# Optimization experiments

Hardware: AMD Instinct MI355X
Metric: run time of the kernel (lower is better)

Reference implementation:

```python
import jax, jax.numpy as jnp
import numpy as np

H = 8
NUM_GRAPHS = 128
EDGE_DIM = 147

def _glorot(k, shape, fan_in):
    return jax.random.normal(k, shape, jnp.float32) * (1.0 / np.sqrt(fan_in))

def setup_inputs():
    ks = jax.random.split(jax.random.key(0), 28)
    N, E = 50000, 200000
    inp = {}
    inp['x'] = jax.random.normal(ks[0], (N, 64), jnp.float32)
    inp['edge_attr'] = jax.random.uniform(ks[1], (E, EDGE_DIM), dtype=jnp.float32)
    dims = [(64, 64), (512, 64), (512, 32)]  # (in_channels, per-head out) per GATConv layer
    ki = 2
    for i in range(3):
        cin, c = dims[i]
        hc = H * c
        inp['W%d' % i] = _glorot(ks[ki], (hc, cin), cin); ki += 1
        inp['We%d' % i] = _glorot(ks[ki], (hc, EDGE_DIM), EDGE_DIM); ki += 1
        inp['as%d' % i] = _glorot(ks[ki], (1, H, c), c); ki += 1
        inp['ad%d' % i] = _glorot(ks[ki], (1, H, c), c); ki += 1
        inp['ae%d' % i] = _glorot(ks[ki], (1, H, c), c); ki += 1
        inp['b%d' % i] = jnp.zeros((hc,), jnp.float32); ki += 1
    inp['Wc'] = _glorot(ks[ki], (32, 256), 256)
    inp['bc'] = jnp.zeros((32,), jnp.float32)
    inp['edge_index'] = jax.random.randint(ks[ki + 1], (2, E), 0, N)
    inp['batch'] = jnp.sort(jax.random.randint(ks[ki + 2], (N,), 0, NUM_GRAPHS))
    return inp

def _gat_layer(x, src, dst, ea, W, We, a_s, a_d, a_e, b):
    # PyG GATConv (concat=True, eval mode): project, per-edge attention logits,
    # softmax over incoming edges of each destination node, weighted scatter-sum, bias.
    N = x.shape[0]
    HC = W.shape[0]
    C = HC // H
    xp = (x @ W.T).reshape(N, H, C)              # [N,H,C]
    ep = (ea @ We.T).reshape(-1, H, C)           # [E,H,C]
    logits = (xp * a_s).sum(-1)[src] + (xp * a_d).sum(-1)[dst] + (ep * a_e).sum(-1)
    logits = jax.nn.leaky_relu(logits, 0.2)      # [E,H]
    mx = jax.ops.segment_max(logits, dst, num_segments=N)
    mx = jnp.where(jnp.isfinite(mx), mx, 0.0)
    ex = jnp.exp(logits - mx[dst])
    denom = jax.ops.segment_sum(ex, dst, num_segments=N)
    attn = ex / (denom[dst] + 1e-16)             # [E,H]
    out = jax.ops.segment_sum(xp[src] * attn[:, :, None], dst, num_segments=N)
    return out.reshape(N, HC) + b

def _forward(x, edge_attr, params, Wc, bc, edge_index, batch):
    N = x.shape[0]
    src, dst = edge_index[0], edge_index[1]
    # GATConv add_self_loops=True, fill_value='mean': self-loop edge attr is
    # the per-node mean of incoming edge attrs (0 for isolated nodes).
    ones_e = jnp.ones((src.shape[0],), x.dtype)
    deg = jax.ops.segment_sum(ones_e, dst, num_segments=N)
    loop_attr = jax.ops.segment_sum(edge_attr, dst, num_segments=N) / jnp.clip(deg, 1.0)[:, None]
    ar = jnp.arange(N)
    src_f = jnp.concatenate([src, ar])
    dst_f = jnp.concatenate([dst, ar])
    ea_f = jnp.concatenate([edge_attr, loop_attr], axis=0)
    h = x
    for i, p in enumerate(params):
        h = _gat_layer(h, src_f, dst_f, ea_f, *p)
        if i < len(params) - 1:
            h = jax.nn.elu(h)  # dropout is identity in eval
    # batch indices are sorted and contiguous, so the unique->contiguous remap
    # in the original forward is the identity; global mean pool:
    cnt = jax.ops.segment_sum(jnp.ones((N,), h.dtype), batch, num_segments=NUM_GRAPHS)
    pooled = jax.ops.segment_sum(h, batch, num_segments=NUM_GRAPHS) / jnp.clip(cnt, 1.0)[:, None]
    return pooled @ Wc.T + bc

def reference(x, edge_attr, W0, We0, as0, ad0, ae0, b0, W1, We1, as1, ad1, ae1, b1, W2, We2, as2, ad2, ae2, b2, Wc, bc, edge_index, batch):
    params = [(W0, We0, as0, ad0, ae0, b0), (W1, We1, as1, ad1, ae1, b1), (W2, We2, as2, ad2, ae2, b2)]
    return _forward(x, edge_attr, params, Wc, bc, edge_index, batch)
```

## Files before the change

kernel.cpp:

```cpp
#include <hip/hip_runtime.h>
#include <hip/hip_bf16.h>
#include <math.h>

typedef __attribute__((ext_vector_type(8))) _Float16 f16x8;
typedef __attribute__((ext_vector_type(4))) _Float16 f16x4;
typedef __attribute__((ext_vector_type(4))) float f32x4;

#define AS1(p) ((const __attribute__((address_space(1))) void*)(p))
#define AS3(p) ((__attribute__((address_space(3))) void*)(p))

__device__ __forceinline__ float leaky02(float x){ return x > 0.f ? x : 0.2f*x; }
__device__ __forceinline__ ushort f2h(float f){ _Float16 h = (_Float16)f; return *(ushort*)&h; }
__device__ __forceinline__ float h2f(ushort u){ _Float16 h = *(_Float16*)&u; return (float)h; }

__global__ void count_kernel(const int* __restrict__ dst, int* __restrict__ cnt, int E){
  int e = blockIdx.x*blockDim.x + threadIdx.x;
  if (e < E) atomicAdd(&cnt[dst[e]], 1);
}

__global__ void scanA_kernel(const int* __restrict__ cnt, int* __restrict__ bsum, int N){
  __shared__ int sd[256];
  int i = blockIdx.x*256 + threadIdx.x;
  sd[threadIdx.x] = (i<N) ? cnt[i] : 0;
  __syncthreads();
  for (int off=128; off>0; off>>=1){
    if (threadIdx.x < off) sd[threadIdx.x] += sd[threadIdx.x+off];
    __syncthreads();
  }
  if (threadIdx.x==0) bsum[blockIdx.x] = sd[0];
}
__global__ void scanB_kernel(int* __restrict__ bsum, int B){
  __shared__ int sd[256];
  int t = threadIdx.x;
  int v = (t<B) ? bsum[t] : 0;
  sd[t] = v;
  __syncthreads();
  for (int off=1; off<256; off<<=1){
    int u = (t>=off) ? sd[t-off] : 0;
    __syncthreads();
    sd[t] += u;
    __syncthreads();
  }
  if (t<B) bsum[t] = sd[t] - v;
}
__global__ void scanC_kernel(const int* __restrict__ cnt, const int* __restrict__ bsum,
                             int* __restrict__ row_ptr, int N){
  __shared__ int sd[256];
  int i = blockIdx.x*256 + threadIdx.x;
  int v = (i<N) ? cnt[i] : 0;
  sd[threadIdx.x] = v;
  __syncthreads();
  for (int off=1; off<256; off<<=1){
    int u = (threadIdx.x>=off) ? sd[threadIdx.x-off] : 0;
    __syncthreads();
    sd[threadIdx.x] += u;
    __syncthreads();
  }
  if (i < N) row_ptr[i+1] = sd[threadIdx.x] + bsum[blockIdx.x];
  if (i == 0) row_ptr[0] = 0;
}

__global__ void scatter_kernel(const int* __restrict__ src, const int* __restrict__ dst,
                               const int* __restrict__ row_ptr, int* __restrict__ cursor,
                               int* __restrict__ epos, int* __restrict__ csr_src,
                               int* __restrict__ csr_dst, int E){
  int e = blockIdx.x*blockDim.x + threadIdx.x;
  if (e < E){
    int d = dst[e];
    int pos = row_ptr[d] + atomicAdd(&cursor[d], 1);
    epos[e] = pos;
    csr_src[pos] = src[e];
    csr_dst[pos] = d;
  }
}

__global__ void conv4_kernel(const float* __restrict__ p0, const float* __restrict__ p1,
                             const float* __restrict__ p2, const float* __restrict__ p3,
                             ushort* __restrict__ q0, ushort* __restrict__ q1,
                             ushort* __restrict__ q2, ushort* __restrict__ q3,
                             int n0, int n1, int n2, int n3){
  int i = blockIdx.x*256 + threadIdx.x;
  const float* src; ushort* dst; int loc;
  if (i < n0){ src=p0; dst=q0; loc=i; }
  else if (i < n0+n1){ src=p1; dst=q1; loc=i-n0; }
  else if (i < n0+n1+n2){ src=p2; dst=q2; loc=i-n0-n1; }
  else if (i < n0+n1+n2+n3){ src=p3; dst=q3; loc=i-n0-n1-n2; }
  else return;
  float4 v = reinterpret_cast<const float4*>(src)[loc];
  ushort4 o; o.x=f2h(v.x); o.y=f2h(v.y); o.z=f2h(v.z); o.w=f2h(v.w);
  reinterpret_cast<ushort4*>(dst)[loc] = o;
}

__global__ void wfold_direct_kernel(const float* __restrict__ We0, const float* __restrict__ ae0,
                                    const float* __restrict__ We1, const float* __restrict__ ae1,
                                    const float* __restrict__ We2, const float* __restrict__ ae2,
                                    ushort* __restrict__ Bh){
  int t = blockIdx.x*256 + threadIdx.x;
  if (t >= 32*160) return;
  int j = t/160, d = t%160;
  float s = 0.f;
  if (j < 24 && d < 147){
    int l = j >> 3, h = j & 7;
    const float* We = (l==0) ? We0 : (l==1) ? We1 : We2;
    const float* ae = (l==0) ? ae0 : (l==1) ? ae1 : ae2;
    int C = (l==2) ? 32 : 64;
    for (int c=0;c<C;c++) s = fmaf(We[(size_t)(h*C+c)*147 + d], ae[h*C+c], s);
  }
  Bh[t] = f2h(s);
}

__global__ __launch_bounds__(256) void edge_alpha_mfma_kernel(const float* __restrict__ ea, const ushort* __restrict__ Bh,
                                                              const int* __restrict__ epos,
                                                              float* __restrict__ aEc, int E){
  int wave = threadIdx.x>>6, lane = threadIdx.x&63;
  int fr = lane&15, fq = lane>>4;
  int m0 = blockIdx.x*64 + wave*16;
  f32x4 acc0 = {0.f,0.f,0.f,0.f}, acc1 = {0.f,0.f,0.f,0.f};
  int row = m0 + fr; if (row > E-1) row = E-1;
  const float*  ar = ea + (size_t)row*147;
  const ushort* b0 = Bh + (size_t)fr*160      + fq*8;
  const ushort* b1 = Bh + (size_t)(16+fr)*160 + fq*8;
  #pragma unroll
  for (int k=0;k<160;k+=32){
    int c0 = k + fq*8;
    f16x8 a;
    #pragma unroll
    for (int u=0;u<8;u++){
      float v = (c0+u < 147) ? ar[c0+u] : 0.f;
      a[u] = (_Float16)v;
    }
    f16x8 p = *(const f16x8*)(b0 + k);
    f16x8 q = *(const f16x8*)(b1 + k);
    acc0 = __builtin_amdgcn_mfma_f32_16x16x32_f16(a, p, acc0, 0, 0, 0);
    acc1 = __builtin_amdgcn_mfma_f32_16x16x32_f16(a, q, acc1, 0, 0, 0);
  }
  #pragma unroll
  for (int j=0;j<4;j++){
    int r = m0 + fq*4 + j;
    if (r < E){
      int p = epos[r];
      aEc[(size_t)p*24 + fr] = acc0[j];
      if (fr < 8) aEc[(size_t)p*24 + 16 + fr] = acc1[j];
    }
  }
}

__global__ __launch_bounds__(192) void loop_alpha_all_kernel(const float* __restrict__ aEc, const int* __restrict__ row_ptr,
                                                             float* __restrict__ loopAE, int N){
  int n = blockIdx.x*8 + threadIdx.x/24;
  int j = threadIdx.x%24;
  if (n >= N) return;
  int row = row_ptr[n], end = row_ptr[n+1];
  float s = 0.f;
  for (int i=row;i<end;i++) s += aEc[(size_t)i*24 + j];
  loopAE[(size_t)n*24 + j] = s / fmaxf((float)(end-row), 1.0f);
}

__global__ __launch_bounds__(256) void edge_exp_kernel(
    const float* __restrict__ alphaS, const float* __restrict__ alphaD,
    const float* __restrict__ aEc, const float* __restrict__ loopAE,
    const int* __restrict__ csr_src, const int* __restrict__ csr_dst,
    float* __restrict__ exv_csr, float* __restrict__ selfEx,
    int E, int N, int off){
  int t = blockIdx.x*256 + threadIdx.x;
  if (t < E*8){
    int i = t >> 3, h = t & 7;
    int s = csr_src[i], n = csr_dst[i];
    float v = leaky02(alphaS[(size_t)s*8+h] + alphaD[(size_t)n*8+h] + aEc[(size_t)i*24 + off + h]);
    exv_csr[t] = __expf(v);
  } else if (t < (E+N)*8){
    int u = t - E*8;
    int n = u >> 3, h = u & 7;
    float v = leaky02(alphaS[(size_t)n*8+h] + alphaD[(size_t)n*8+h] + loopAE[(size_t)n*24 + off + h]);
    selfEx[u] = __expf(v);
  }
}

template<int CPH>
__global__ __launch_bounds__(256) void gemm_mfma_kernel(const ushort* __restrict__ A, const ushort* __restrict__ B,
                                                        ushort* __restrict__ C,
                                                        const float* __restrict__ a_s, const float* __restrict__ a_d,
                                                        float* __restrict__ alphaS, float* __restrict__ alphaD,
                                                        int M, int Nn, int K, int NY){
  __shared__ ushort lds[128*64*4];
  int nwg = gridDim.x;
  int bid = blockIdx.x;
  int q8 = nwg >> 3, r8 = nwg & 7;
  int xcd = bid & 7, loc = bid >> 3;
  int swz = (xcd < r8 ? xcd*(q8+1) : r8*(q8+1) + (xcd-r8)*q8) + loc;
  int m0 = (swz / NY) * 128, n0 = (swz % NY) * 128;

  int wave = threadIdx.x >> 6, lane = threadIdx.x & 63;
  int wr = wave >> 1, wc = wave & 1;
  f32x4 acc[4][4];
  #pragma unroll
  for (int m=0;m<4;m++)
    #pragma unroll
    for (int n=0;n<4;n++) acc[m][n] = (f32x4){0.f,0.f,0.f,0.f};

  int lrow = lane >> 3;
  int lcol = lane & 7;
  int srcChunk = lcol ^ lrow;
  int fr = lane & 15;
  int fq = lane >> 4;

  auto stage = [&](int buf, int k0){
    ushort* As = lds + buf*(128*64*2);
    ushort* Bs = As + 128*64;
    #pragma unroll
    for (int qq=0;qq<4;qq++){
      int r = qq*32 + wave*8 + lrow;
      int gr = m0 + r; if (gr > M-1) gr = M-1;
      __builtin_amdgcn_global_load_lds(AS1(A + (size_t)gr*K + k0 + srcChunk*8), AS3(&As[(qq*32 + wave*8)*64]), 16, 0, 0);
      __builtin_amdgcn_global_load_lds(AS1(B + (size_t)(n0 + r)*K + k0 + srcChunk*8), AS3(&Bs[(qq*32 + wave*8)*64]), 16, 0, 0);
    }
  };

  int nt = K >> 6;
  stage(0, 0);
  int buf = 0;
  for (int t=0; t<nt; ++t){
    if (t+1 < nt){
      stage(buf^1, (t+1)<<6);
      asm volatile("s_waitcnt vmcnt(8)" ::: "memory");
    } else {
      asm volatile("s_waitcnt vmcnt(0)" ::: "memory");
    }
    __builtin_amdgcn_s_barrier();
    __builtin_amdgcn_sched_barrier(0);
    const ushort* As = lds + buf*(128*64*2);
    const ushort* Bs = As + 128*64;
    #pragma unroll
    for (int kk=0; kk<64; kk+=32){
      f16x8 a[4], b[4];
      #pragma unroll
      for (int m=0;m<4;m++){
        int Ra = wr*64 + m*16 + fr;
        int ch = ((kk>>3) + fq) ^ (Ra & 7);
        a[m] = *(const f16x8*)&As[Ra*64 + ch*8];
      }
      #pragma unroll
      for (int n=0;n<4;n++){
        int Rb = wc*64 + n*16 + fr;
        int ch = ((kk>>3) + fq) ^ (Rb & 7);
        b[n] = *(const f16x8*)&Bs[Rb*64 + ch*8];
      }
      #pragma unroll
      for (int m=0;m<4;m++)
        #pragma unroll
        for (int n=0;n<4;n++)
          acc[m][n] = __builtin_amdgcn_mfma_f32_16x16x32_f16(a[m], b[n], acc[m][n], 0, 0, 0);
    }
    __builtin_amdgcn_s_barrier();
    buf ^= 1;
  }

  {
    ushort* Cs = lds;
    #pragma unroll
    for (int m=0;m<4;m++)
      #pragma unroll
      for (int j=0;j<4;j++){
        int rr = wr*64 + m*16 + fq*4 + j;
        #pragma unroll
        for (int n=0;n<4;n++)
          Cs[rr*128 + wc*64 + n*16 + fr] = f2h(acc[m][n][j]);
      }
    __builtin_amdgcn_s_barrier();
    int rbase = threadIdx.x >> 4;
    int cc = (threadIdx.x & 15)*8;
    #pragma unroll
    for (int p=0;p<8;p++){
      int rr = p*16 + rbase;
      int grow = m0 + rr;
      if (grow < M)
        *(f16x8*)(C + (size_t)grow*Nn + n0 + cc) = *(const f16x8*)&Cs[rr*128 + cc];
    }
  }

  int colbase = n0 + wc*64;
  if (CPH == 64){
    int head = colbase >> 6;
    float asv[4], adv[4];
    #pragma unroll
    for (int n=0;n<4;n++){ int cih = n*16 + fr; asv[n] = a_s[head*64 + cih]; adv[n] = a_d[head*64 + cih]; }
    #pragma unroll
    for (int m=0;m<4;m++){
      float ps[4] = {0,0,0,0}, pd[4] = {0,0,0,0};
      #pragma unroll
      for (int n=0;n<4;n++)
        #pragma unroll
        for (int j=0;j<4;j++){ ps[j] = fmaf(acc[m][n][j], asv[n], ps[j]); pd[j] = fmaf(acc[m][n][j], adv[n], pd[j]); }
      #pragma unroll
      for (int off=1; off<16; off<<=1)
        #pragma unroll
        for (int j=0;j<4;j++){ ps[j] += __shfl_xor(ps[j], off); pd[j] += __shfl_xor(pd[j], off); }
      if (fr == 0){
        #pragma unroll
        for (int j=0;j<4;j++){
          int row = m0 + wr*64 + m*16 + fq*4 + j;
          if (row < M){ alphaS[(size_t)row*8 + head] = ps[j]; alphaD[(size_t)row*8 + head] = pd[j]; }
        }
      }
    }
  } else {
    int head0 = colbase >> 5;
    float asv[4], adv[4];
    #pragma unroll
    for (int n=0;n<4;n++){
      int h = head0 + (n>>1);
      int cih = (n&1)*16 + fr;
      asv[n] = a_s[h*32 + cih]; adv[n] = a_d[h*32 + cih];
    }
    #pragma unroll
    for (int m=0;m<4;m++){
      float psA[4]={0,0,0,0}, pdA[4]={0,0,0,0}, psB[4]={0,0,0,0}, pdB[4]={0,0,0,0};
      #pragma unroll
      for (int j=0;j<4;j++){
        #pragma unroll
        for (int n=0;n<2;n++){ psA[j] = fmaf(acc[m][n][j], asv[n], psA[j]); pdA[j] = fmaf(acc[m][n][j], adv[n], pdA[j]); }
        #pragma unroll
        for (int n=2;n<4;n++){ psB[j] = fmaf(acc[m][n][j], asv[n], psB[j]); pdB[j] = fmaf(acc[m][n][j], adv[n], pdB[j]); }
      }
      #pragma unroll
      for (int off=1; off<16; off<<=1)
        #pragma unroll
        for (int j=0;j<4;j++){
          psA[j] += __shfl_xor(psA[j], off); pdA[j] += __shfl_xor(pdA[j], off);
          psB[j] += __shfl_xor(psB[j], off); pdB[j] += __shfl_xor(pdB[j], off);
        }
      if (fr == 0){
        #pragma unroll
        for (int j=0;j<4;j++){
          int row = m0 + wr*64 + m*16 + fq*4 + j;
          if (row < M){
            alphaS[(size_t)row*8 + head0]     = psA[j]; alphaD[(size_t)row*8 + head0]     = pdA[j];
            alphaS[(size_t)row*8 + head0 + 1] = psB[j]; alphaD[(size_t)row*8 + head0 + 1] = pdB[j];
          }
        }
      }
    }
  }
}

template<int V>
__device__ __forceinline__ void rowfma(const ushort* p, float ex, float* acc){
  if (V == 8){
    f16x8 v = *(const f16x8*)p;
    #pragma unroll
    for (int j=0;j<8;j++) acc[j] = fmaf(ex, (float)v[j], acc[j]);
  } else {
    f16x4 v = *(const f16x4*)p;
    #pragma unroll
    for (int j=0;j<V;j++) acc[j] = fmaf(ex, (float)v[j], acc[j]);
  }
}

template<int HC, int ELU>
__global__ __launch_bounds__(256) void aggregate_kernel(
    const ushort* __restrict__ xh, const float* __restrict__ exv_csr, const float* __restrict__ selfEx,
    const int* __restrict__ row_ptr, const int* __restrict__ csr_src,
    const float* __restrict__ bias, ushort* __restrict__ out, int N){
  constexpr int V = HC/64;
  int w = blockIdx.x*4 + (threadIdx.x>>6);
  int nA = w*2, nB = w*2+1;
  if (nA >= N) return;
  bool hasB = (nB < N);
  int lane = threadIdx.x & 63;
  int h = lane >> 3;
  int cofs = V*lane;

  float accA[V], accB[V];
  float exsA = selfEx[(size_t)nA*8 + h];
  float denA = exsA;
  {
    const ushort* xr = xh + (size_t)nA*HC + cofs;
    #pragma unroll
    for (int j=0;j<V;j++) accA[j] = 0.f;
    rowfma<V>(xr, exsA, accA);
  }
  float denB = 0.f;
  #pragma unroll
  for (int j=0;j<V;j++) accB[j] = 0.f;
  int iA = row_ptr[nA], eA = row_ptr[nA+1];
  int iB = eA, eB = eA;
  if (hasB){
    float exsB = selfEx[(size_t)nB*8 + h];
    denB = exsB;
    rowfma<V>(xh + (size_t)nB*HC + cofs, exsB, accB);
    eB = row_ptr[nB+1];
  }

  while (iA+1 < eA && iB+1 < eB){
    int sA0 = csr_src[iA],  sA1 = csr_src[iA+1];
    int sB0 = csr_src[iB],  sB1 = csr_src[iB+1];
    float exA0 = exv_csr[(size_t)iA*8 + h],     exA1 = exv_csr[(size_t)(iA+1)*8 + h];
    float exB0 = exv_csr[(size_t)iB*8 + h],     exB1 = exv_csr[(size_t)(iB+1)*8 + h];
    const ushort* pA0 = xh + (size_t)sA0*HC + cofs;
    const ushort* pA1 = xh + (size_t)sA1*HC + cofs;
    const ushort* pB0 = xh + (size_t)sB0*HC + cofs;
    const ushort* pB1 = xh + (size_t)sB1*HC + cofs;
    denA += exA0 + exA1; denB += exB0 + exB1;
    rowfma<V>(pA0, exA0, accA);
    rowfma<V>(pA1, exA1, accA);
    rowfma<V>(pB0, exB0, accB);
    rowfma<V>(pB1, exB1, accB);
    iA += 2; iB += 2;
  }
  for (; iA+1 < eA; iA += 2){
    int s0 = csr_src[iA], s1 = csr_src[iA+1];
    float ex0 = exv_csr[(size_t)iA*8 + h], ex1 = exv_csr[(size_t)(iA+1)*8 + h];
    const ushort* p0 = xh + (size_t)s0*HC + cofs;
    const ushort* p1 = xh + (size_t)s1*HC + cofs;
    denA += ex0 + ex1;
    rowfma<V>(p0, ex0, accA);
    rowfma<V>(p1, ex1, accA);
  }
  if (iA < eA){
    int s = csr_src[iA];
    float ex = exv_csr[(size_t)iA*8 + h];
    denA += ex;
    rowfma<V>(xh + (size_t)s*HC + cofs, ex, accA);
  }
  for (; iB+1 < eB; iB += 2){
    int s0 = csr_src[iB], s1 = csr_src[iB+1];
    float ex0 = exv_csr[(size_t)iB*8 + h], ex1 = exv_csr[(size_t)(iB+1)*8 + h];
    const ushort* p0 = xh + (size_t)s0*HC + cofs;
    const ushort* p1 = xh + (size_t)s1*HC + cofs;
    denB += ex0 + ex1;
    rowfma<V>(p0, ex0, accB);
    rowfma<V>(p1, ex1, accB);
  }
  if (iB < eB){
    int s = csr_src[iB];
    float ex = exv_csr[(size_t)iB*8 + h];
    denB += ex;
    rowfma<V>(xh + (size_t)s*HC + cofs, ex, accB);
  }

  float invA = 1.f/(denA + 1e-16f);
  {
    if (V == 8){
      f16x8 ov;
      #pragma unroll
      for (int j=0;j<8;j++){
        float o = accA[j]*invA + bias[cofs + j];
        if (ELU) o = (o > 0.f) ? o : (__expf(o) - 1.f);
        ov[j] = (_Float16)o;
      }
      *(f16x8*)(out + (size_t)nA*HC + cofs) = ov;
    } else {
      f16x4 ov;
      #pragma unroll
      for (int j=0;j<V;j++){
        float o = accA[j]*invA + bias[cofs + j];
        if (ELU) o = (o > 0.f) ? o : (__expf(o) - 1.f);
        ov[j] = (_Float16)o;
      }
      *(f16x4*)(out + (size_t)nA*HC + cofs) = ov;
    }
  }
  if (hasB){
    float invB = 1.f/(denB + 1e-16f);
    if (V == 8){
      f16x8 ov;
      #pragma unroll
      for (int j=0;j<8;j++){
        float o = accB[j]*invB + bias[cofs + j];
        if (ELU) o = (o > 0.f) ? o : (__expf(o) - 1.f);
        ov[j] = (_Float16)o;
      }
      *(f16x8*)(out + (size_t)nB*HC + cofs) = ov;
    } else {
      f16x4 ov;
      #pragma unroll
      for (int j=0;j<V;j++){
        float o = accB[j]*invB + bias[cofs + j];
        if (ELU) o = (o > 0.f) ? o : (__expf(o) - 1.f);
        ov[j] = (_Float16)o;
      }
      *(f16x4*)(out + (size_t)nB*HC + cofs) = ov;
    }
  }
}

__global__ __launch_bounds__(256) void pool_sum_kernel(const ushort* __restrict__ h, const int* __restrict__ batch,
                                                       float* __restrict__ pooled, int N){
  __shared__ int bsh[128];
  int i0 = blockIdx.x*128;
  int i1 = min(i0+128, N);
  if (threadIdx.x < i1-i0) bsh[threadIdx.x] = batch[i0+threadIdx.x];
  __syncthreads();
  int c = threadIdx.x;
  int gprev = bsh[0];
  float s = 0.f;
  for (int i=i0;i<i1;i++){
    int g = bsh[i-i0];
    if (g != gprev){ atomicAdd(&pooled[gprev*256 + c], s); s = 0.f; gprev = g; }
    s += h2f(h[(size_t)i*256 + c]);
  }
  atomicAdd(&pooled[gprev*256 + c], s);
}

__device__ __forceinline__ int lower_bound_i(const int* a, int n, int key){
  int lo=0, hi=n;
  while (lo<hi){ int mid=(lo+hi)>>1; if (a[mid]<key) lo=mid+1; else hi=mid; }
  return lo;
}

__global__ void final_kernel(const float* __restrict__ pooled, const int* __restrict__ batch,
                             const float* __restrict__ Wc, const float* __restrict__ bc,
                             float* __restrict__ out, int N){
  int g = blockIdx.x; int j = threadIdx.x;
  if (j >= 32) return;
  int start = lower_bound_i(batch, N, g);
  int end   = lower_bound_i(batch, N, g+1);
  float invc = 1.f / fmaxf((float)(end-start), 1.f);
  const float* p = pooled + g*256;
  const float* w = Wc + (size_t)j*256;
  float s = 0.f;
  for (int c=0;c<256;c++) s = fmaf(p[c], w[c], s);
  out[g*32 + j] = s*invc + bc[j];
}

extern "C" void kernel_launch(void* const* d_in, const int* in_sizes, int n_in,
                              void* d_out, int out_size, void* d_ws, size_t ws_size,
                              hipStream_t stream){
  (void)n_in; (void)out_size; (void)ws_size;
  const float* x   = (const float*)d_in[0];
  const float* ea  = (const float*)d_in[1];
  const float* Wt[3]  = {(const float*)d_in[2],  (const float*)d_in[8],  (const float*)d_in[14]};
  const float* Wet[3] = {(const float*)d_in[3],  (const float*)d_in[9],  (const float*)d_in[15]};
  const float* ast[3] = {(const float*)d_in[4],  (const float*)d_in[10], (const float*)d_in[16]};
  const float* adt[3] = {(const float*)d_in[5],  (const float*)d_in[11], (const float*)d_in[17]};
  const float* aet[3] = {(const float*)d_in[6],  (const float*)d_in[12], (const float*)d_in[18]};
  const float* bt[3]  = {(const float*)d_in[7],  (const float*)d_in[13], (const float*)d_in[19]};
  const float* Wc  = (const float*)d_in[20];
  const float* bc  = (const float*)d_in[21];
  const int* ei    = (const int*)d_in[22];
  const int* batch = (const int*)d_in[23];
  int N = in_sizes[0] / 64;
  int E = in_sizes[1] / 147;
  const int* srcp = ei;
  const int* dstp = ei + E;

  char* w = (char*)d_ws;
  size_t off = 0;
  auto carve = [&](size_t bytes)->char*{ char* p = w + off; off += (bytes + 255) & ~(size_t)255; return p; };
  ushort* xh     = (ushort*)carve((size_t)N*512*2);
  ushort* hb     = (ushort*)carve((size_t)N*512*2);
  ushort* xb     = (ushort*)carve((size_t)N*64*2);
  ushort* Wb[3];
  Wb[0] = (ushort*)carve((size_t)512*64*2);
  Wb[1] = (ushort*)carve((size_t)512*512*2);
  Wb[2] = (ushort*)carve((size_t)256*512*2);
  ushort* wfBh   = (ushort*)carve((size_t)32*160*2);
  float*  aEc    = (float*) carve((size_t)E*24*4);
  float*  loopAE = (float*) carve((size_t)N*24*4);
  float*  alphaS = (float*) carve((size_t)N*8*4);
  float*  alphaD = (float*) carve((size_t)N*8*4);
  float*  exv    = (float*) carve((size_t)E*8*4);
  float*  selfEx = (float*) carve((size_t)N*8*4);
  int*    row_ptr= (int*)   carve((size_t)(N+1)*4);
  int*    epos   = (int*)   carve((size_t)E*4);
  int*    csr_src= (int*)   carve((size_t)E*4);
  int*    csr_dst= (int*)   carve((size_t)E*4);
  int*    bsum   = (int*)   carve((size_t)256*4);
  char*   zbase  = carve(0);
  float*  pooled = (float*) carve((size_t)128*256*4);
  int*    cnt    = (int*)   carve((size_t)N*4);
  int*    cursor = (int*)   carve((size_t)N*4);
  char*   zend   = carve(0);

  hipMemsetAsync(zbase, 0, (size_t)(zend - zbase), stream);

  int nscan = (N+255)/256;
  count_kernel  <<<(E+255)/256, 256, 0, stream>>>(dstp, cnt, E);
  scanA_kernel  <<<nscan, 256, 0, stream>>>(cnt, bsum, N);
  scanB_kernel  <<<1, 256, 0, stream>>>(bsum, nscan);
  scanC_kernel  <<<nscan, 256, 0, stream>>>(cnt, bsum, row_ptr, N);
  scatter_kernel<<<(E+255)/256, 256, 0, stream>>>(srcp, dstp, row_ptr, cursor, epos, csr_src, csr_dst, E);

  wfold_direct_kernel<<<(32*160+255)/256, 256, 0, stream>>>(Wet[0], aet[0], Wet[1], aet[1], Wet[2], aet[2], wfBh);

  conv4_kernel<<<(N*16 + 8192 + 65536 + 32768 + 255)/256, 256, 0, stream>>>(
      x, Wt[0], Wt[1], Wt[2], xb, Wb[0], Wb[1], Wb[2], N*16, 8192, 65536, 32768);

  edge_alpha_mfma_kernel<<<(E+63)/64, 256, 0, stream>>>(ea, wfBh, epos, aEc, E);
  loop_alpha_all_kernel <<<(N+7)/8, 192, 0, stream>>>(aEc, row_ptr, loopAE, N);

  const int HCs[3]  = {512, 512, 256};
  const int CINs[3] = {64, 512, 512};
  int nrow = (N+127)/128;
  int nexp = ((E+N)*8 + 255)/256;
  for (int l=0; l<3; l++){
    int HC = HCs[l], CIN = CINs[l];
    const ushort* Ain = (l==0) ? xb : hb;
    int NY = HC/128;
    int nwg = nrow * NY;
    if (HC==512) gemm_mfma_kernel<64><<<nwg, 256, 0, stream>>>(Ain, Wb[l], xh, ast[l], adt[l], alphaS, alphaD, N, HC, CIN, NY);
    else         gemm_mfma_kernel<32><<<nwg, 256, 0, stream>>>(Ain, Wb[l], xh, ast[l], adt[l], alphaS, alphaD, N, HC, CIN, NY);
    edge_exp_kernel<<<nexp, 256, 0, stream>>>(alphaS, alphaD, aEc, loopAE, csr_src, csr_dst, exv, selfEx, E, N, l*8);
    int ablocks = (N + 7) / 8;
    if (l==0)
      aggregate_kernel<512,1><<<ablocks, 256, 0, stream>>>(xh, exv, selfEx, row_ptr, csr_src, bt[l], hb, N);
    else if (l==1)
      aggregate_kernel<512,1><<<ablocks, 256, 0, stream>>>(xh, exv, selfEx, row_ptr, csr_src, bt[l], hb, N);
    else
      aggregate_kernel<256,0><<<ablocks, 256, 0, stream>>>(xh, exv, selfEx, row_ptr, csr_src, bt[l], hb, N);
  }
  pool_sum_kernel<<<(N+127)/128, 256, 0, stream>>>(hb, batch, pooled, N);
  final_kernel<<<128, 64, 0, stream>>>(pooled, batch, Wc, bc, (float*)d_out, N);
}
```

Measured before the change: 434.3 us.

## Fuse edge attention exp into aggregation kernel with software-pipelined gathers

Removes the per-layer edge_exp kernel and computes leaky-relu/exp attention weights inline inside the aggregation kernel from alphaS, alphaD and aEc. This eliminates the exv/selfEx buffers, the csr_dst array and one launch per layer, along with their global write/read traffic. The main loop is also software-pipelined: it prefetches the next pair of source indices, alpha values and feature rows for both nodes before doing the current FMAs. In exchange it adds register pressure and redundant exp work per lane, since each of the 8 lanes in a head group recomputes the same exp.

```diff
diff --git a/kernel.cpp b/kernel.cpp
--- a/kernel.cpp
+++ b/kernel.cpp
@@ -62,15 +62,13 @@
 
 __global__ void scatter_kernel(const int* __restrict__ src, const int* __restrict__ dst,
                                const int* __restrict__ row_ptr, int* __restrict__ cursor,
-                               int* __restrict__ epos, int* __restrict__ csr_src,
-                               int* __restrict__ csr_dst, int E){
+                               int* __restrict__ epos, int* __restrict__ csr_src, int E){
   int e = blockIdx.x*blockDim.x + threadIdx.x;
   if (e < E){
     int d = dst[e];
     int pos = row_ptr[d] + atomicAdd(&cursor[d], 1);
     epos[e] = pos;
     csr_src[pos] = src[e];
-    csr_dst[pos] = d;
   }
 }
 
@@ -156,26 +154,6 @@
   loopAE[(size_t)n*24 + j] = s / fmaxf((float)(end-row), 1.0f);
 }
 
-__global__ __launch_bounds__(256) void edge_exp_kernel(
-    const float* __restrict__ alphaS, const float* __restrict__ alphaD,
-    const float* __restrict__ aEc, const float* __restrict__ loopAE,
-    const int* __restrict__ csr_src, const int* __restrict__ csr_dst,
-    float* __restrict__ exv_csr, float* __restrict__ selfEx,
-    int E, int N, int off){
-  int t = blockIdx.x*256 + threadIdx.x;
-  if (t < E*8){
-    int i = t >> 3, h = t & 7;
-    int s = csr_src[i], n = csr_dst[i];
-    float v = leaky02(alphaS[(size_t)s*8+h] + alphaD[(size_t)n*8+h] + aEc[(size_t)i*24 + off + h]);
-    exv_csr[t] = __expf(v);
-  } else if (t < (E+N)*8){
-    int u = t - E*8;
-    int n = u >> 3, h = u & 7;
-    float v = leaky02(alphaS[(size_t)n*8+h] + alphaD[(size_t)n*8+h] + loopAE[(size_t)n*24 + off + h]);
-    selfEx[u] = __expf(v);
-  }
-}
-
 template<int CPH>
 __global__ __launch_bounds__(256) void gemm_mfma_kernel(const ushort* __restrict__ A, const ushort* __restrict__ B,
                                                         ushort* __restrict__ C,
@@ -343,25 +321,24 @@
   }
 }
 
+template<int V> struct vecT;
+template<> struct vecT<8>{ typedef f16x8 T; };
+template<> struct vecT<4>{ typedef f16x4 T; };
+
 template<int V>
-__device__ __forceinline__ void rowfma(const ushort* p, float ex, float* acc){
-  if (V == 8){
-    f16x8 v = *(const f16x8*)p;
-    #pragma unroll
-    for (int j=0;j<8;j++) acc[j] = fmaf(ex, (float)v[j], acc[j]);
-  } else {
-    f16x4 v = *(const f16x4*)p;
-    #pragma unroll
-    for (int j=0;j<V;j++) acc[j] = fmaf(ex, (float)v[j], acc[j]);
-  }
+__device__ __forceinline__ void rowfma(typename vecT<V>::T v, float ex, float* acc){
+  #pragma unroll
+  for (int j=0;j<V;j++) acc[j] = fmaf(ex, (float)v[j], acc[j]);
 }
 
 template<int HC, int ELU>
 __global__ __launch_bounds__(256) void aggregate_kernel(
-    const ushort* __restrict__ xh, const float* __restrict__ exv_csr, const float* __restrict__ selfEx,
+    const ushort* __restrict__ xh, const float* __restrict__ alphaS, const float* __restrict__ alphaD,
+    const float* __restrict__ aEc, const float* __restrict__ loopAE,
     const int* __restrict__ row_ptr, const int* __restrict__ csr_src,
-    const float* __restrict__ bias, ushort* __restrict__ out, int N){
+    const float* __restrict__ bias, ushort* __restrict__ out, int N, int off){
   constexpr int V = HC/64;
+  typedef typename vecT<V>::T vec;
   int w = blockIdx.x*4 + (threadIdx.x>>6);
   int nA = w*2, nB = w*2+1;
   if (nA >= N) return;
@@ -370,117 +347,127 @@
   int h = lane >> 3;
   int cofs = V*lane;
 
+  float adnA = alphaD[(size_t)nA*8 + h];
   float accA[V], accB[V];
-  float exsA = selfEx[(size_t)nA*8 + h];
-  float denA = exsA;
+  float denA, denB = 0.f;
   {
-    const ushort* xr = xh + (size_t)nA*HC + cofs;
+    float exs = __expf(leaky02(alphaS[(size_t)nA*8 + h] + adnA + loopAE[(size_t)nA*24 + off + h]));
+    denA = exs;
     #pragma unroll
     for (int j=0;j<V;j++) accA[j] = 0.f;
-    rowfma<V>(xr, exsA, accA);
-  }
-  float denB = 0.f;
+    rowfma<V>(*(const vec*)(xh + (size_t)nA*HC + cofs), exs, accA);
+  }
   #pragma unroll
   for (int j=0;j<V;j++) accB[j] = 0.f;
-  int iA = row_ptr[nA], eA = row_ptr[nA+1];
-  int iB = eA, eB = eA;
+  float adnB = 0.f;
+  int iA = row_ptr[nA], eAe = row_ptr[nA+1];
+  int iB = eAe, eBe = eAe;
   if (hasB){
-    float exsB = selfEx[(size_t)nB*8 + h];
-    denB = exsB;
-    rowfma<V>(xh + (size_t)nB*HC + cofs, exsB, accB);
-    eB = row_ptr[nB+1];
-  }
-
-  while (iA+1 < eA && iB+1 < eB){
-    int sA0 = csr_src[iA],  sA1 = csr_src[iA+1];
-    int sB0 = csr_src[iB],  sB1 = csr_src[iB+1];
-    float exA0 = exv_csr[(size_t)iA*8 + h],     exA1 = exv_csr[(size_t)(iA+1)*8 + h];
-    float exB0 = exv_csr[(size_t)iB*8 + h],     exB1 = exv_csr[(size_t)(iB+1)*8 + h];
-    const ushort* pA0 = xh + (size_t)sA0*HC + cofs;
-    const ushort* pA1 = xh + (size_t)sA1*HC + cofs;
-    const ushort* pB0 = xh + (size_t)sB0*HC + cofs;
-    const ushort* pB1 = xh + (size_t)sB1*HC + cofs;
-    denA += exA0 + exA1; denB += exB0 + exB1;
-    rowfma<V>(pA0, exA0, accA);
-    rowfma<V>(pA1, exA1, accA);
-    rowfma<V>(pB0, exB0, accB);
-    rowfma<V>(pB1, exB1, accB);
-    iA += 2; iB += 2;
-  }
-  for (; iA+1 < eA; iA += 2){
+    adnB = alphaD[(size_t)nB*8 + h];
+    float exs = __expf(leaky02(alphaS[(size_t)nB*8 + h] + adnB + loopAE[(size_t)nB*24 + off + h]));
+    denB = exs;
+    rowfma<V>(*(const vec*)(xh + (size_t)nB*HC + cofs), exs, accB);
+    eBe = row_ptr[nB+1];
+  }
+
+  bool run = (iA+1 < eAe) && (iB+1 < eBe);
+  int sA0=0,sA1=0,sB0=0,sB1=0;
+  float gA0=0,gA1=0,gB0=0,gB1=0, tA0=0,tA1=0,tB0=0,tB1=0;
+  vec vA0{}, vA1{}, vB0{}, vB1{};
+  if (run){
+    sA0=csr_src[iA]; sA1=csr_src[iA+1]; sB0=csr_src[iB]; sB1=csr_src[iB+1];
+    gA0=alphaS[(size_t)sA0*8+h]; gA1=alphaS[(size_t)sA1*8+h];
+    gB0=alphaS[(size_t)sB0*8+h]; gB1=alphaS[(size_t)sB1*8+h];
+    tA0=aEc[(size_t)iA*24+off+h]; tA1=aEc[(size_t)(iA+1)*24+off+h];
+    tB0=aEc[(size_t)iB*24+off+h]; tB1=aEc[(size_t)(iB+1)*24+off+h];
+    vA0=*(const vec*)(xh+(size_t)sA0*HC+cofs); vA1=*(const vec*)(xh+(size_t)sA1*HC+cofs);
+    vB0=*(const vec*)(xh+(size_t)sB0*HC+cofs); vB1=*(const vec*)(xh+(size_t)sB1*HC+cofs);
+  }
+  while (run){
+    int jA = iA+2, jB = iB+2;
+    bool nrun = (jA+1 < eAe) && (jB+1 < eBe);
+    vec cA0=vA0, cA1=vA1, cB0=vB0, cB1=vB1;
+    float eA0=__expf(leaky02(gA0+adnA+tA0));
+    float eA1=__expf(leaky02(gA1+adnA+tA1));
+    float eB0=__expf(leaky02(gB0+adnB+tB0));
+    float eB1=__expf(leaky02(gB1+adnB+tB1));
+    if (nrun){
+      sA0=csr_src[jA]; sA1=csr_src[jA+1]; sB0=csr_src[jB]; sB1=csr_src[jB+1];
+      gA0=alphaS[(size_t)sA0*8+h]; gA1=alphaS[(size_t)sA1*8+h];
+      gB0=alphaS[(size_t)sB0*8+h]; gB1=alphaS[(size_t)sB1*8+h];
+      tA0=aEc[(size_t)jA*24+off+h]; tA1=aEc[(size_t)(jA+1)*24+off+h];
+      tB0=aEc[(size_t)jB*24+off+h]; tB1=aEc[(size_t)(jB+1)*24+off+h];
+      vA0=*(const vec*)(xh+(size_t)sA0*HC+cofs); vA1=*(const vec*)(xh+(size_t)sA1*HC+cofs);
+      vB0=*(const vec*)(xh+(size_t)sB0*HC+cofs); vB1=*(const vec*)(xh+(size_t)sB1*HC+cofs);
+    }
+    denA += eA0 + eA1; denB += eB0 + eB1;
+    rowfma<V>(cA0, eA0, accA); rowfma<V>(cA1, eA1, accA);
+    rowfma<V>(cB0, eB0, accB); rowfma<V>(cB1, eB1, accB);
+    iA = jA; iB = jB;
+    run = nrun;
+  }
+  for (; iA+1 < eAe; iA += 2){
     int s0 = csr_src[iA], s1 = csr_src[iA+1];
-    float ex0 = exv_csr[(size_t)iA*8 + h], ex1 = exv_csr[(size_t)(iA+1)*8 + h];
-    const ushort* p0 = xh + (size_t)s0*HC + cofs;
-    const ushort* p1 = xh + (size_t)s1*HC + cofs;
-    denA += ex0 + ex1;
-    rowfma<V>(p0, ex0, accA);
-    rowfma<V>(p1, ex1, accA);
-  }
-  if (iA < eA){
+    float g0 = alphaS[(size_t)s0*8+h], g1 = alphaS[(size_t)s1*8+h];
+    float t0 = aEc[(size_t)iA*24+off+h], t1 = aEc[(size_t)(iA+1)*24+off+h];
+    vec v0 = *(const vec*)(xh+(size_t)s0*HC+cofs);
+    vec v1 = *(const vec*)(xh+(size_t)s1*HC+cofs);
+    float e0 = __expf(leaky02(g0+adnA+t0));
+    float e1 = __expf(leaky02(g1+adnA+t1));
+    denA += e0 + e1;
+    rowfma<V>(v0, e0, accA); rowfma<V>(v1, e1, accA);
+  }
+  if (iA < eAe){
     int s = csr_src[iA];
-    float ex = exv_csr[(size_t)iA*8 + h];
-    denA += ex;
-    rowfma<V>(xh + (size_t)s*HC + cofs, ex, accA);
-  }
-  for (; iB+1 < eB; iB += 2){
+    float g = alphaS[(size_t)s*8+h];
+    float t = aEc[(size_t)iA*24+off+h];
+    vec v = *(const vec*)(xh+(size_t)s*HC+cofs);
+    float e = __expf(leaky02(g+adnA+t));
+    denA += e;
+    rowfma<V>(v, e, accA);
+  }
+  for (; iB+1 < eBe; iB += 2){
     int s0 = csr_src[iB], s1 = csr_src[iB+1];
-    float ex0 = exv_csr[(size_t)iB*8 + h], ex1 = exv_csr[(size_t)(iB+1)*8 + h];
-    const ushort* p0 = xh + (size_t)s0*HC + cofs;
-    const ushort* p1 = xh + (size_t)s1*HC + cofs;
-    denB += ex0 + ex1;
-    rowfma<V>(p0, ex0, accB);
-    rowfma<V>(p1, ex1, accB);
-  }
-  if (iB < eB){
+    float g0 = alphaS[(size_t)s0*8+h], g1 = alphaS[(size_t)s1*8+h];
+    float t0 = aEc[(size_t)iB*24+off+h], t1 = aEc[(size_t)(iB+1)*24+off+h];
+    vec v0 = *(const vec*)(xh+(size_t)s0*HC+cofs);
+    vec v1 = *(const vec*)(xh+(size_t)s1*HC+cofs);
+    float e0 = __expf(leaky02(g0+adnB+t0));
+    float e1 = __expf(leaky02(g1+adnB+t1));
+    denB += e0 + e1;
+    rowfma<V>(v0, e0, accB); rowfma<V>(v1, e1, accB);
+  }
+  if (iB < eBe){
     int s = csr_src[iB];
-    float ex = exv_csr[(size_t)iB*8 + h];
-    denB += ex;
-    rowfma<V>(xh + (size_t)s*HC + cofs, ex, accB);
+    float g = alphaS[(size_t)s*8+h];
+    float t = aEc[(size_t)iB*24+off+h];
+    vec v = *(const vec*)(xh+(size_t)s*HC+cofs);
+    float e = __expf(leaky02(g+adnB+t));
+    denB += e;
+    rowfma<V>(v, e, accB);
   }
 
   float invA = 1.f/(denA + 1e-16f);
   {
-    if (V == 8){
-      f16x8 ov;
-      #pragma unroll
-      for (int j=0;j<8;j++){
-        float o = accA[j]*invA + bias[cofs + j];
-        if (ELU) o = (o > 0.f) ? o : (__expf(o) - 1.f);
-        ov[j] = (_Float16)o;
-      }
-      *(f16x8*)(out + (size_t)nA*HC + cofs) = ov;
-    } else {
-      f16x4 ov;
-      #pragma unroll
-      for (int j=0;j<V;j++){
-        float o = accA[j]*invA + bias[cofs + j];
-        if (ELU) o = (o > 0.f) ? o : (__expf(o) - 1.f);
-        ov[j] = (_Float16)o;
-      }
-      *(f16x4*)(out + (size_t)nA*HC + cofs) = ov;
-    }
+    vec ov;
+    #pragma unroll
+    for (int j=0;j<V;j++){
+      float o = accA[j]*invA + bias[cofs + j];
+      if (ELU) o = (o > 0.f) ? o : (__expf(o) - 1.f);
+      ov[j] = (_Float16)o;
+    }
+    *(vec*)(out + (size_t)nA*HC + cofs) = ov;
   }
   if (hasB){
     float invB = 1.f/(denB + 1e-16f);
-    if (V == 8){
-      f16x8 ov;
-      #pragma unroll
-      for (int j=0;j<8;j++){
-        float o = accB[j]*invB + bias[cofs + j];
-        if (ELU) o = (o > 0.f) ? o : (__expf(o) - 1.f);
-        ov[j] = (_Float16)o;
-      }
-      *(f16x8*)(out + (size_t)nB*HC + cofs) = ov;
-    } else {
-      f16x4 ov;
-      #pragma unroll
-      for (int j=0;j<V;j++){
-        float o = accB[j]*invB + bias[cofs + j];
-        if (ELU) o = (o > 0.f) ? o : (__expf(o) - 1.f);
-        ov[j] = (_Float16)o;
-      }
-      *(f16x4*)(out + (size_t)nB*HC + cofs) = ov;
-    }
+    vec ov;
+    #pragma unroll
+    for (int j=0;j<V;j++){
+      float o = accB[j]*invB + bias[cofs + j];
+      if (ELU) o = (o > 0.f) ? o : (__expf(o) - 1.f);
+      ov[j] = (_Float16)o;
+    }
+    *(vec*)(out + (size_t)nB*HC + cofs) = ov;
   }
 }
 
@@ -559,12 +546,9 @@
   float*  loopAE = (float*) carve((size_t)N*24*4);
   float*  alphaS = (float*) carve((size_t)N*8*4);
   float*  alphaD = (float*) carve((size_t)N*8*4);
-  float*  exv    = (float*) carve((size_t)E*8*4);
-  float*  selfEx = (float*) carve((size_t)N*8*4);
   int*    row_ptr= (int*)   carve((size_t)(N+1)*4);
   int*    epos   = (int*)   carve((size_t)E*4);
   int*    csr_src= (int*)   carve((size_t)E*4);
-  int*    csr_dst= (int*)   carve((size_t)E*4);
   int*    bsum   = (int*)   carve((size_t)256*4);
   char*   zbase  = carve(0);
   float*  pooled = (float*) carve((size_t)128*256*4);
@@ -579,7 +563,7 @@
   scanA_kernel  <<<nscan, 256, 0, stream>>>(cnt, bsum, N);
   scanB_kernel  <<<1, 256, 0, stream>>>(bsum, nscan);
   scanC_kernel  <<<nscan, 256, 0, stream>>>(cnt, bsum, row_ptr, N);
-  scatter_kernel<<<(E+255)/256, 256, 0, stream>>>(srcp, dstp, row_ptr, cursor, epos, csr_src, csr_dst, E);
+  scatter_kernel<<<(E+255)/256, 256, 0, stream>>>(srcp, dstp, row_ptr, cursor, epos, csr_src, E);
 
   wfold_direct_kernel<<<(32*160+255)/256, 256, 0, stream>>>(Wet[0], aet[0], Wet[1], aet[1], Wet[2], aet[2], wfBh);
 
@@ -592,7 +576,6 @@
   const int HCs[3]  = {512, 512, 256};
   const int CINs[3] = {64, 512, 512};
   int nrow = (N+127)/128;
-  int nexp = ((E+N)*8 + 255)/256;
   for (int l=0; l<3; l++){
     int HC = HCs[l], CIN = CINs[l];
     const ushort* Ain = (l==0) ? xb : hb;
@@ -600,14 +583,13 @@
     int nwg = nrow * NY;
     if (HC==512) gemm_mfma_kernel<64><<<nwg, 256, 0, stream>>>(Ain, Wb[l], xh, ast[l], adt[l], alphaS, alphaD, N, HC, CIN, NY);
     else         gemm_mfma_kernel<32><<<nwg, 256, 0, stream>>>(Ain, Wb[l], xh, ast[l], adt[l], alphaS, alphaD, N, HC, CIN, NY);
-    edge_exp_kernel<<<nexp, 256, 0, stream>>>(alphaS, alphaD, aEc, loopAE, csr_src, csr_dst, exv, selfEx, E, N, l*8);
     int ablocks = (N + 7) / 8;
     if (l==0)
-      aggregate_kernel<512,1><<<ablocks, 256, 0, stream>>>(xh, exv, selfEx, row_ptr, csr_src, bt[l], hb, N);
+      aggregate_kernel<512,1><<<ablocks, 256, 0, stream>>>(xh, alphaS, alphaD, aEc, loopAE, row_ptr, csr_src, bt[l], hb, N, 0);
     else if (l==1)
-      aggregate_kernel<512,1><<<ablocks, 256, 0, stream>>>(xh, exv, selfEx, row_ptr, csr_src, bt[l], hb, N);
+      aggregate_kernel<512,1><<<ablocks, 256, 0, stream>>>(xh, alphaS, alphaD, aEc, loopAE, row_ptr, csr_src, bt[l], hb, N, 8);
     else
-      aggregate_kernel<256,0><<<ablocks, 256, 0, stream>>>(xh, exv, selfEx, row_ptr, csr_src, bt[l], hb, N);
+      aggregate_kernel<256,0><<<ablocks, 256, 0, stream>>>(xh, alphaS, alphaD, aEc, loopAE, row_ptr, csr_src, bt[l], hb, N, 16);
   }
   pool_sum_kernel<<<(N+127)/128, 256, 0, stream>>>(hb, batch, pooled, N);
   final_kernel<<<128, 64, 0, stream>>>(pooled, batch, Wc, bc, (float*)d_out, N);
```

New measurement: 423.7 us. -2.4%, faster.
